# Optimization experiments

Hardware: AMD Instinct MI355X
Metric: run time of the kernel (lower is better)

Reference implementation:

```python
import jax, jax.numpy as jnp
import numpy as np

NUM_HEADS = 32
NUM_KV_HEADS = 8
HEAD_DIM = 128
HIDDEN = 4096
EPS = 1e-6
ROPE_BASE = 10000.0
NEG_INF = -1e9


def setup_inputs() -> dict:
    key = jax.random.key(0)
    ks = jax.random.split(key, 6)
    B, S = 1, 2048
    hidden_states = jax.random.normal(ks[0], (B, S, HIDDEN), dtype=jnp.float32)
    wq = jax.random.normal(ks[1], (HIDDEN, NUM_HEADS * HEAD_DIM), dtype=jnp.float32) * 0.02
    wk = jax.random.normal(ks[2], (HIDDEN, NUM_KV_HEADS * HEAD_DIM), dtype=jnp.float32) * 0.02
    wv = jax.random.normal(ks[3], (HIDDEN, NUM_KV_HEADS * HEAD_DIM), dtype=jnp.float32) * 0.02
    wo = jax.random.normal(ks[4], (NUM_HEADS * HEAD_DIM, HIDDEN), dtype=jnp.float32) * 0.02
    q_norm_w = jnp.ones((HEAD_DIM,), dtype=jnp.float32)
    k_norm_w = jnp.ones((HEAD_DIM,), dtype=jnp.float32)
    attention_mask = jnp.tril(jnp.ones((S, S), dtype=bool))[None, None]  # [1,1,S,S] causal allow-mask
    position_ids = jnp.arange(S, dtype=jnp.int64 if jax.config.jax_enable_x64 else jnp.int32)[None, :]
    return dict(hidden_states=hidden_states, wq=wq, wk=wk, wv=wv, wo=wo,
                q_norm_w=q_norm_w, k_norm_w=k_norm_w,
                attention_mask=attention_mask, position_ids=position_ids)


def _rotate_half(x):
    x1, x2 = jnp.split(x, 2, axis=-1)
    return jnp.concatenate((-x2, x1), axis=-1)


def _rms_norm(x, w):
    xf = x.astype(jnp.float32)
    var = jnp.mean(xf * xf, axis=-1, keepdims=True)
    return w * (xf * jax.lax.rsqrt(var + EPS)).astype(x.dtype)


def reference(hidden_states, wq, wk, wv, wo, q_norm_w, k_norm_w, attention_mask, position_ids):
    B, S, _ = hidden_states.shape
    dtype = hidden_states.dtype

    # projections -> [B, H, S, D]
    q = (hidden_states @ wq).reshape(B, S, NUM_HEADS, HEAD_DIM).transpose(0, 2, 1, 3)
    k = (hidden_states @ wk).reshape(B, S, NUM_KV_HEADS, HEAD_DIM).transpose(0, 2, 1, 3)
    v = (hidden_states @ wv).reshape(B, S, NUM_KV_HEADS, HEAD_DIM).transpose(0, 2, 1, 3)

    # RoPE cache (fp32), gathered by position_ids
    inv_freq = 1.0 / (ROPE_BASE ** (jnp.arange(0, HEAD_DIM, 2, dtype=jnp.float32) / HEAD_DIM))
    t = jnp.arange(S, dtype=jnp.float32)
    freqs = jnp.outer(t, inv_freq)                    # [S, D/2]
    emb = jnp.concatenate((freqs, freqs), axis=-1)    # [S, D]
    cos = jnp.cos(emb).astype(dtype)[position_ids][:, None]  # [B,1,S,D]
    sin = jnp.sin(emb).astype(dtype)[position_ids][:, None]

    q = q * cos + _rotate_half(q) * sin
    k = k * cos + _rotate_half(k) * sin

    # QK RMSNorm (after RoPE)
    q = _rms_norm(q, q_norm_w)
    k = _rms_norm(k, k_norm_w)

    # GQA repeat-kv
    n_rep = NUM_HEADS // NUM_KV_HEADS
    k = jnp.repeat(k, n_rep, axis=1)
    v = jnp.repeat(v, n_rep, axis=1)

    scores = jnp.einsum('bhqd,bhkd->bhqk', q, k) / np.sqrt(HEAD_DIM)
    scores = jnp.where(attention_mask, scores, scores + NEG_INF)
    probs = jax.nn.softmax(scores.astype(jnp.float32), axis=-1).astype(dtype)
    out = jnp.einsum('bhqk,bhkd->bhqd', probs, v)      # [B,H,S,D]
    out = out.transpose(0, 2, 1, 3).reshape(B, S, NUM_HEADS * HEAD_DIM)
    return out @ wo
```

## Files before the change

kernel.cpp:

```cpp
#include <hip/hip_runtime.h>

typedef __bf16 bf16x8 __attribute__((ext_vector_type(8)));
typedef float f32x4 __attribute__((ext_vector_type(4)));
typedef unsigned short u16x8 __attribute__((ext_vector_type(8)));
typedef unsigned short u16x4 __attribute__((ext_vector_type(4)));
typedef unsigned short u16x2 __attribute__((ext_vector_type(2)));

__device__ inline unsigned short f2bf(float f) {
    return __builtin_bit_cast(unsigned short, (__bf16)f);
}
__device__ inline float bf2f(unsigned short u) {
    return (float)__builtin_bit_cast(__bf16, u);
}

__device__ __forceinline__ float fexp2(float x) {
    float r;
    asm("v_exp_f32 %0, %1" : "=v"(r) : "v"(x));
    return r;
}

__device__ inline void storeC(float v, float* p) { *p = v; }
__device__ inline void storeC(float v, unsigned short* p) { *p = f2bf(v); }

#define MFMA16(a, b, c) __builtin_amdgcn_mfma_f32_16x16x32_bf16( \
    __builtin_bit_cast(bf16x8, a), __builtin_bit_cast(bf16x8, b), (c), 0, 0, 0)

__device__ inline void gload16(const unsigned short* g, unsigned short* l) {
    __builtin_amdgcn_global_load_lds(
        (const __attribute__((address_space(1))) unsigned int*)(g),
        (__attribute__((address_space(3))) unsigned int*)(l), 16, 0, 0);
}

__device__ __forceinline__ void bar() {
    asm volatile("" ::: "memory");
    __builtin_amdgcn_s_barrier();
    asm volatile("" ::: "memory");
}
#define WAITVM(N) asm volatile("s_waitcnt vmcnt(" #N ")" ::: "memory")

__device__ void transpose_tile128(const float* __restrict__ W,
                                  unsigned short* __restrict__ WT,
                                  int K, int N, int bx, int by,
                                  unsigned short* t_lds)
{
    constexpr int LDT = 130;
    const int kt = bx * 128, nt = by * 128;
    const int tid = threadIdx.x;
    const int c = (tid & 31) * 4;
    const int r0 = tid >> 5;
    #pragma unroll
    for (int p = 0; p < 16; ++p) {
        const int r = p * 8 + r0;
        float4 v = *(const float4*)&W[(size_t)(kt + r) * N + nt + c];
        u16x4 h;
        h[0] = f2bf(v.x); h[1] = f2bf(v.y); h[2] = f2bf(v.z); h[3] = f2bf(v.w);
        *(u16x4*)&t_lds[r * LDT + c] = h;
    }
    __syncthreads();
    const int kc = (tid >> 4) * 8;
    const int n0 = tid & 15;
    #pragma unroll
    for (int p = 0; p < 8; ++p) {
        const int n = p * 16 + n0;
        u16x8 o;
        #pragma unroll
        for (int j = 0; j < 8; ++j)
            o[j] = t_lds[(kc + j) * LDT + n];
        const int swz = (kc & 64) | ((kc & 63) ^ ((n & 7) << 3));
        *(u16x8*)&WT[(size_t)(nt + n) * K + kt + swz] = o;
    }
}

__global__ __launch_bounds__(256) void prep_all(
    const float* __restrict__ hidden, const float* __restrict__ wq,
    const float* __restrict__ wk, const float* __restrict__ wv,
    const float* __restrict__ wo, unsigned short* __restrict__ hb,
    unsigned short* __restrict__ wqt, unsigned short* __restrict__ wkt,
    unsigned short* __restrict__ wot)
{
    __shared__ __attribute__((aligned(16))) unsigned short t_lds[128 * 130];
    const int bid = blockIdx.x;
    if (bid < 4096) {
        const size_t i = ((size_t)bid * 256 + threadIdx.x) * 8;
        const size_t row7 = (i >> 12) & 7;
        float4 v0 = *(const float4*)&hidden[i];
        float4 v1 = *(const float4*)&hidden[i + 4];
        u16x8 o;
        o[0] = f2bf(v0.x); o[1] = f2bf(v0.y); o[2] = f2bf(v0.z); o[3] = f2bf(v0.w);
        o[4] = f2bf(v1.x); o[5] = f2bf(v1.y); o[6] = f2bf(v1.z); o[7] = f2bf(v1.w);
        *(u16x8*)&hb[i ^ (row7 << 3)] = o;
    } else if (bid < 5120) {
        const int tb = bid - 4096;
        transpose_tile128(wq, wqt, 4096, 4096, tb & 31, tb >> 5, t_lds);
    } else if (bid < 5376) {
        const int tb = bid - 5120;
        transpose_tile128(wk, wkt, 4096, 1024, tb & 31, tb >> 5, t_lds);
    } else if (bid < 5632) {
        const int tb = bid - 5376;
        transpose_tile128(wv, wkt + (size_t)1024 * 4096, 4096, 1024,
                          tb & 31, tb >> 5, t_lds);
    } else {
        const int tb = bid - 5632;
        transpose_tile128(wo, wot, 4096, 4096, tb & 31, tb >> 5, t_lds);
    }
}

template <typename CT, int CMODE>
__global__ __launch_bounds__(512) void gemm8(
    const unsigned short* __restrict__ A, const unsigned short* __restrict__ B,
    CT* __restrict__ C, int M, int N, int K)
{
    constexpr int ASZ = 128 * 64, BSZ = 256 * 64;
    __shared__ __attribute__((aligned(16))) unsigned short a_lds[3 * ASZ];
    __shared__ __attribute__((aligned(16))) unsigned short b_lds[3 * BSZ];

    const int bm0 = blockIdx.y * 128, bn0 = blockIdx.x * 256;
    const int tid = threadIdx.x, lane = tid & 63, wid = tid >> 6;
    const int wr = wid >> 2, wc = wid & 3;
    const int l15 = lane & 15, koff = (lane >> 4) * 8;
    const int sw = (l15 & 7) << 3;
    const int cb0 = koff ^ sw;
    const int cb1 = (32 + koff) ^ sw;

    f32x4 acc[4][4] = {};

    const size_t kbase = (CMODE == 3) ? (size_t)blockIdx.z * 2048 : 0;

    const unsigned short* ag[2];
    const unsigned short* bg[4];
    #pragma unroll
    for (int p = 0; p < 2; ++p) {
        const int row = (wid + p * 8) * 8 + (lane >> 3);
        ag[p] = A + (size_t)(bm0 + row) * K + (lane & 7) * 8 + kbase;
    }
    #pragma unroll
    for (int p = 0; p < 4; ++p) {
        const int row = (wid + p * 8) * 8 + (lane >> 3);
        bg[p] = B + (size_t)(bn0 + row) * K + (lane & 7) * 8 + kbase;
    }

    const int nt = (CMODE == 3) ? 32 : (K >> 6);

    auto stageA = [&](int s, int kt, int p) {
        gload16(ag[p] + kt, a_lds + s * ASZ + (wid + p * 8) * 512);
    };
    auto stageB = [&](int s, int kt, int p) {
        gload16(bg[p] + kt, b_lds + s * BSZ + (wid + p * 8) * 512);
    };

    #pragma unroll
    for (int p = 0; p < 2; ++p) stageA(0, 0, p);
    #pragma unroll
    for (int p = 0; p < 4; ++p) stageB(0, 0, p);
    #pragma unroll
    for (int p = 0; p < 2; ++p) stageA(1, 64, p);
    #pragma unroll
    for (int p = 0; p < 4; ++p) stageB(1, 64, p);
    WAITVM(6);
    bar();

    int sc = 0;
    for (int t = 0; t < nt; ++t) {
        const unsigned short* ab = a_lds + sc * ASZ;
        const unsigned short* bb = b_lds + sc * BSZ;
        const int ss = (sc >= 1) ? sc - 1 : 2;
        const int kt2 = (t + 2) << 6;
        const bool st = (t + 2) < nt;

        u16x8 af0, af1, af2, af3, bfr[4];

        af0 = *(const u16x8*)&ab[(wr * 64 + 0 * 16 + l15) * 64 + cb0];
        af1 = *(const u16x8*)&ab[(wr * 64 + 1 * 16 + l15) * 64 + cb0];
        af2 = *(const u16x8*)&ab[(wr * 64 + 2 * 16 + l15) * 64 + cb0];
        af3 = *(const u16x8*)&ab[(wr * 64 + 3 * 16 + l15) * 64 + cb0];
        #pragma unroll
        for (int j = 0; j < 4; ++j)
            bfr[j] = *(const u16x8*)&bb[(wc * 64 + j * 16 + l15) * 64 + cb0];
        if (st) { stageA(ss, kt2, 0); stageA(ss, kt2, 1); stageB(ss, kt2, 0); }
        bar();
        __builtin_amdgcn_s_setprio(1);
        #pragma unroll
        for (int j = 0; j < 4; ++j) {
            acc[0][j] = MFMA16(af0, bfr[j], acc[0][j]);
            acc[1][j] = MFMA16(af1, bfr[j], acc[1][j]);
            acc[2][j] = MFMA16(af2, bfr[j], acc[2][j]);
            acc[3][j] = MFMA16(af3, bfr[j], acc[3][j]);
        }
        __builtin_amdgcn_s_setprio(0);

        af0 = *(const u16x8*)&ab[(wr * 64 + 0 * 16 + l15) * 64 + cb1];
        af1 = *(const u16x8*)&ab[(wr * 64 + 1 * 16 + l15) * 64 + cb1];
        af2 = *(const u16x8*)&ab[(wr * 64 + 2 * 16 + l15) * 64 + cb1];
        af3 = *(const u16x8*)&ab[(wr * 64 + 3 * 16 + l15) * 64 + cb1];
        #pragma unroll
        for (int j = 0; j < 4; ++j)
            bfr[j] = *(const u16x8*)&bb[(wc * 64 + j * 16 + l15) * 64 + cb1];
        if (st) {
            stageB(ss, kt2, 1); stageB(ss, kt2, 2); stageB(ss, kt2, 3);
            WAITVM(6);
        } else {
            WAITVM(0);
        }
        bar();
        __builtin_amdgcn_s_setprio(1);
        #pragma unroll
        for (int j = 0; j < 4; ++j) {
            acc[0][j] = MFMA16(af0, bfr[j], acc[0][j]);
            acc[1][j] = MFMA16(af1, bfr[j], acc[1][j]);
            acc[2][j] = MFMA16(af2, bfr[j], acc[2][j]);
            acc[3][j] = MFMA16(af3, bfr[j], acc[3][j]);
        }
        __builtin_amdgcn_s_setprio(0);

        bar();
        sc = (sc == 2) ? 0 : sc + 1;
    }

    CT* Cb = C;
    if constexpr (CMODE == 3)
        Cb = C + (size_t)blockIdx.z * M * N;

    #pragma unroll
    for (int i = 0; i < 4; ++i)
        #pragma unroll
        for (int r = 0; r < 4; ++r) {
            const int row = bm0 + wr * 64 + i * 16 + (lane >> 4) * 4 + r;
            size_t base = (size_t)row * N + bn0 + wc * 64 + l15;
            #pragma unroll
            for (int j = 0; j < 4; ++j)
                storeC(acc[i][j][r], &Cb[base + j * 16]);
        }
}

__global__ __launch_bounds__(256) void combine_kv(
    const float* __restrict__ P, unsigned short* __restrict__ Kout,
    unsigned short* __restrict__ VTout)
{
    const float* P0 = P;
    const float* P1 = P + (size_t)2048 * 2048;
    const int s0 = blockIdx.y * 64, c0 = blockIdx.x * 64;
    const int tid = threadIdx.x;
    const int row = tid >> 2;
    const int cbl = (tid & 3) * 16;
    const size_t gbase = (size_t)(s0 + row) * 2048 + c0 + cbl;
    u16x8 o[2];
    #pragma unroll
    for (int j = 0; j < 2; ++j) {
        float4 a0 = *(const float4*)&P0[gbase + j * 8];
        float4 b0 = *(const float4*)&P1[gbase + j * 8];
        float4 a1 = *(const float4*)&P0[gbase + j * 8 + 4];
        float4 b1 = *(const float4*)&P1[gbase + j * 8 + 4];
        o[j][0] = f2bf(a0.x + b0.x); o[j][1] = f2bf(a0.y + b0.y);
        o[j][2] = f2bf(a0.z + b0.z); o[j][3] = f2bf(a0.w + b0.w);
        o[j][4] = f2bf(a1.x + b1.x); o[j][5] = f2bf(a1.y + b1.y);
        o[j][6] = f2bf(a1.z + b1.z); o[j][7] = f2bf(a1.w + b1.w);
    }
    if (c0 < 1024) {
        #pragma unroll
        for (int j = 0; j < 2; ++j)
            *(u16x8*)&Kout[(size_t)(s0 + row) * 1024 + c0 + cbl + j * 8] = o[j];
    } else {
        constexpr int LDT = 66;
        __shared__ unsigned short t_lds[64 * LDT];
        #pragma unroll
        for (int j = 0; j < 2; ++j)
            *(u16x8*)&t_lds[row * LDT + cbl + j * 8] = o[j];
        __syncthreads();
        const int d = row;
        #pragma unroll
        for (int j = 0; j < 2; ++j) {
            u16x8 w;
            #pragma unroll
            for (int e = 0; e < 8; ++e)
                w[e] = t_lds[(cbl + j * 8 + e) * LDT + d];
            *(u16x8*)&VTout[(size_t)(c0 - 1024 + d) * 2048 + s0 + cbl + j * 8] = w;
        }
    }
}

__device__ void rope_row(unsigned short* __restrict__ X,
                         const float* __restrict__ W,
                         float fpos, int rowstride, size_t s, int h, int t8,
                         float outscale)
{
    unsigned short* p = X + s * rowstride + h * 128 + t8 * 8;
    u16x8 lo = *(u16x8*)p;
    u16x8 hi = *(u16x8*)(p + 64);
    float na[8], nb[8];
    float ss = 0.f;
    #pragma unroll
    for (int j = 0; j < 8; ++j) {
        const int d = t8 * 8 + j;
        float inv = expf(-0.14391156831212787f * (float)d);
        float fr = fpos * inv;
        float c = cosf(fr), sn = sinf(fr);
        float a = bf2f(lo[j]), b = bf2f(hi[j]);
        na[j] = a * c - b * sn;
        nb[j] = b * c + a * sn;
        ss += na[j] * na[j] + nb[j] * nb[j];
    }
    ss += __shfl_xor(ss, 1, 8);
    ss += __shfl_xor(ss, 2, 8);
    ss += __shfl_xor(ss, 4, 8);
    const float rn = rsqrtf(ss * (1.0f / 128.0f) + 1e-6f) * outscale;
    #pragma unroll
    for (int j = 0; j < 8; ++j) {
        const int d = t8 * 8 + j;
        lo[j] = f2bf(na[j] * rn * W[d]);
        hi[j] = f2bf(nb[j] * rn * W[d + 64]);
    }
    *(u16x8*)p = lo;
    *(u16x8*)(p + 64) = hi;
}

__global__ void rope_all(unsigned short* __restrict__ Q,
                         unsigned short* __restrict__ K,
                         const int* __restrict__ pos_ids,
                         const float* __restrict__ qw,
                         const float* __restrict__ kw,
                         float qscale)
{
    const int bid = blockIdx.x;
    const int tid = threadIdx.x;
    if (bid < 2048) {
        rope_row(Q, qw, (float)pos_ids[bid], 4096, (size_t)bid,
                 tid >> 3, tid & 7, qscale);
    } else {
        const size_t s = (size_t)(bid - 2048) * 4 + (tid >> 6);
        rope_row(K, kw, (float)pos_ids[s], 1024, s,
                 (tid & 63) >> 3, tid & 7, 1.0f);
    }
}

__global__ __launch_bounds__(256, 2) void attn_kernel(
    const unsigned short* __restrict__ Q, const unsigned short* __restrict__ K,
    const unsigned short* __restrict__ VT, unsigned short* __restrict__ O)
{
    constexpr int LDK = 136, LDV = 72, LDP = 72;
    __shared__ __attribute__((aligned(16))) unsigned short k_lds[64 * LDK];
    __shared__ __attribute__((aligned(16))) unsigned short v_lds[128 * LDV];
    __shared__ __attribute__((aligned(16))) unsigned short p_lds[4 * 32 * LDP];

    const int bid = blockIdx.x;
    const int kvh = bid & 7;
    const int rest = bid >> 3;
    const int h = kvh * 4 + (rest & 3);
    const int qb = 15 - (rest >> 2);
    const int q0 = qb * 128;
    const int tid = threadIdx.x, lane = tid & 63, wid = tid >> 6;
    const int l15 = lane & 15, g4 = (lane >> 4) * 4, koff = (lane >> 4) * 8;
    const int qw = q0 + wid * 32;

    u16x8 qf[2][4];
    #pragma unroll
    for (int qt = 0; qt < 2; ++qt)
        #pragma unroll
        for (int kk = 0; kk < 4; ++kk)
            qf[qt][kk] = *(const u16x8*)&Q[(size_t)(qw + qt * 16 + l15) * 4096 +
                                           h * 128 + kk * 32 + koff];

    f32x4 o_acc[2][8] = {};
    float m_r[2] = {-1e30f, -1e30f}, l_r[2] = {0.f, 0.f};

    const int kr = tid >> 2, kd = (tid & 3) * 32;
    const int vr = tid >> 1, vc = (tid & 1) * 32;
    const unsigned short* kg = K + (size_t)kvh * 128 + kd;
    const unsigned short* vg = VT + (size_t)(kvh * 128 + vr) * 2048 + vc;

    const int nchunk = qb * 2 + 2;
    u16x8 kst[4], vst[4];
    #pragma unroll
    for (int j = 0; j < 4; ++j) {
        kst[j] = *(const u16x8*)&kg[(size_t)kr * 1024 + j * 8];
        vst[j] = *(const u16x8*)&vg[j * 8];
    }

    for (int ch = 0; ch < nchunk; ++ch) {
        const int kv0 = ch * 64;
        __syncthreads();
        #pragma unroll
        for (int j = 0; j < 4; ++j) {
            *(u16x8*)&k_lds[kr * LDK + kd + j * 8] = kst[j];
            *(u16x8*)&v_lds[vr * LDV + vc + j * 8] = vst[j];
        }
        __syncthreads();
        if (ch + 1 < nchunk) {
            const int kv1 = kv0 + 64;
            #pragma unroll
            for (int j = 0; j < 4; ++j) {
                kst[j] = *(const u16x8*)&kg[(size_t)(kv1 + kr) * 1024 + j * 8];
                vst[j] = *(const u16x8*)&vg[kv1 + j * 8];
            }
        }

        if (kv0 <= qw + 31) {
            f32x4 sacc[2][4] = {};
            #pragma unroll
            for (int kk = 0; kk < 4; ++kk)
                #pragma unroll
                for (int jt = 0; jt < 4; ++jt) {
                    u16x8 kf = *(u16x8*)&k_lds[(jt * 16 + l15) * LDK + kk * 32 + koff];
                    #pragma unroll
                    for (int qt = 0; qt < 2; ++qt)
                        sacc[qt][jt] = MFMA16(kf, qf[qt][kk], sacc[qt][jt]);
                }

            const bool needmask = (kv0 + 63 > qw);
            #pragma unroll
            for (int qt = 0; qt < 2; ++qt) {
                const int q = qw + qt * 16 + l15;
                if (needmask) {
                    #pragma unroll
                    for (int jt = 0; jt < 4; ++jt)
                        #pragma unroll
                        for (int r = 0; r < 4; ++r)
                            if (kv0 + jt * 16 + g4 + r > q) sacc[qt][jt][r] = -1e9f;
                }
                float pmax = sacc[qt][0][0];
                #pragma unroll
                for (int jt = 0; jt < 4; ++jt)
                    #pragma unroll
                    for (int r = 0; r < 4; ++r)
                        pmax = fmaxf(pmax, sacc[qt][jt][r]);
                pmax = fmaxf(pmax, __shfl_xor(pmax, 16));
                pmax = fmaxf(pmax, __shfl_xor(pmax, 32));
                if (__any(pmax > m_r[qt] + 11.5415603f)) {
                    float mnew = fmaxf(m_r[qt], pmax);
                    float alpha = fexp2(m_r[qt] - mnew);
                    m_r[qt] = mnew;
                    l_r[qt] *= alpha;
                    float arow[4];
                    #pragma unroll
                    for (int r = 0; r < 4; ++r)
                        arow[r] = __shfl(alpha, g4 + r, 16);
                    #pragma unroll
                    for (int nt = 0; nt < 8; ++nt)
                        #pragma unroll
                        for (int r = 0; r < 4; ++r)
                            o_acc[qt][nt][r] *= arow[r];
                }
                float ps = 0.f;
                #pragma unroll
                for (int jt = 0; jt < 4; ++jt)
                    #pragma unroll
                    for (int r = 0; r < 4; ++r) {
                        float e = fexp2(sacc[qt][jt][r] - m_r[qt]);
                        sacc[qt][jt][r] = e;
                        ps += e;
                    }
                ps += __shfl_xor(ps, 16);
                ps += __shfl_xor(ps, 32);
                l_r[qt] += ps;
                const int prow = (wid * 32 + qt * 16 + l15) * LDP;
                #pragma unroll
                for (int jt = 0; jt < 4; ++jt) {
                    u16x4 w;
                    #pragma unroll
                    for (int r = 0; r < 4; ++r) w[r] = f2bf(sacc[qt][jt][r]);
                    *(u16x4*)&p_lds[prow + jt * 16 + g4] = w;
                }
            }

            u16x8 pf[2][2];
            #pragma unroll
            for (int qt = 0; qt < 2; ++qt)
                #pragma unroll
                for (int ks = 0; ks < 2; ++ks)
                    pf[qt][ks] = *(u16x8*)&p_lds[(wid * 32 + qt * 16 + l15) * LDP +
                                                 ks * 32 + koff];
            #pragma unroll
            for (int nt = 0; nt < 8; ++nt)
                #pragma unroll
                for (int ks = 0; ks < 2; ++ks) {
                    u16x8 vf = *(u16x8*)&v_lds[(nt * 16 + l15) * LDV + ks * 32 + koff];
                    #pragma unroll
                    for (int qt = 0; qt < 2; ++qt)
                        o_acc[qt][nt] = MFMA16(pf[qt][ks], vf, o_acc[qt][nt]);
                }
        }
    }

    #pragma unroll
    for (int qt = 0; qt < 2; ++qt) {
        float lrow[4];
        #pragma unroll
        for (int r = 0; r < 4; ++r)
            lrow[r] = __shfl(l_r[qt], g4 + r, 16);
        #pragma unroll
        for (int r = 0; r < 4; ++r) {
            float inv_l = 1.0f / lrow[r];
            int row = qw + qt * 16 + g4 + r;
            const int r7s = (row & 7) << 3;
            #pragma unroll
            for (int nt = 0; nt < 8; ++nt) {
                int col = h * 128 + nt * 16 + l15;
                O[(size_t)row * 4096 + (col ^ r7s)] =
                    f2bf(o_acc[qt][nt][r] * inv_l);
            }
        }
    }
}

extern "C" void kernel_launch(void* const* d_in, const int* in_sizes, int n_in,
                              void* d_out, int out_size, void* d_ws, size_t ws_size,
                              hipStream_t stream)
{
    (void)in_sizes; (void)n_in; (void)out_size; (void)ws_size;
    const float* hidden = (const float*)d_in[0];
    const float* wq     = (const float*)d_in[1];
    const float* wk     = (const float*)d_in[2];
    const float* wv     = (const float*)d_in[3];
    const float* wo     = (const float*)d_in[4];
    const float* qnw    = (const float*)d_in[5];
    const float* knw    = (const float*)d_in[6];
    const int*   pos    = (const int*)d_in[8];
    float* out = (float*)d_out;

    const size_t MB = 1024 * 1024;
    char* ws = (char*)d_ws;
    unsigned short* q_ws  = (unsigned short*)(ws);
    unsigned short* k_ws  = (unsigned short*)(ws + 16 * MB);
    unsigned short* vt_ws = (unsigned short*)(ws + 20 * MB);
    unsigned short* hb    = (unsigned short*)(ws + 24 * MB);
    unsigned short* a_ws  = hb;
    unsigned short* wqt   = (unsigned short*)(ws + 40 * MB);
    float*          kvP   = (float*)(ws + 40 * MB);
    unsigned short* wkt   = (unsigned short*)(ws + 72 * MB);
    unsigned short* wot   = (unsigned short*)(ws + 88 * MB);

    prep_all<<<6656, 256, 0, stream>>>(hidden, wq, wk, wv, wo,
                                       hb, wqt, wkt, wot);

    gemm8<unsigned short, 0><<<dim3(16, 16), 512, 0, stream>>>(
        hb, wqt, q_ws, 2048, 4096, 4096);
    gemm8<float, 3><<<dim3(8, 16, 2), 512, 0, stream>>>(
        hb, wkt, kvP, 2048, 2048, 4096);
    combine_kv<<<dim3(32, 32), 256, 0, stream>>>(kvP, k_ws, vt_ws);

    rope_all<<<2560, 256, 0, stream>>>(q_ws, k_ws, pos, qnw, knw,
                                       0.12751743341633942f);

    attn_kernel<<<512, 256, 0, stream>>>(q_ws, k_ws, vt_ws, a_ws);

    gemm8<float, 0><<<dim3(16, 16), 512, 0, stream>>>(
        a_ws, wot, out, 2048, 4096, 4096);
}
```

Measured before the change: 327.1 us.

## Use 256x256 split-K GEMM with partial-sum combine kernels for projections

Adds a new GEMM kernel with 256x256 output tiles, double-buffered LDS and two blocks per CU. It splits K across blockIdx.z and writes fp32 partial sums, which separate combine kernels reduce into bf16 Q, K/V^T, or the fp32 output. The larger tiles raise arithmetic intensity, and split-K supplies enough blocks to fill the CUs. The cost is extra fp32 partial-sum traffic, additional launches, and a dependence on workspace size, with a fallback to the old path when the workspace is too small.

```diff
diff --git a/kernel.cpp b/kernel.cpp
--- a/kernel.cpp
+++ b/kernel.cpp
@@ -102,6 +102,172 @@
     } else {
         const int tb = bid - 5632;
         transpose_tile128(wo, wot, 4096, 4096, tb & 31, tb >> 5, t_lds);
+    }
+}
+
+__global__ __launch_bounds__(512, 2) void gemm256(
+    const unsigned short* __restrict__ A, const unsigned short* __restrict__ B,
+    float* __restrict__ P, int M, int N, int K)
+{
+    constexpr int TSZ = 256 * 64;
+    __shared__ __attribute__((aligned(16))) unsigned short a_lds[2 * TSZ];
+    __shared__ __attribute__((aligned(16))) unsigned short b_lds[2 * TSZ];
+
+    const int bm0 = blockIdx.y * 256, bn0 = blockIdx.x * 256;
+    const int tid = threadIdx.x, lane = tid & 63, wid = tid >> 6;
+    const int wr = wid >> 2, wc = wid & 3;
+    const int l15 = lane & 15, koff = (lane >> 4) * 8;
+    const int sw = (l15 & 7) << 3;
+    const int cb0 = koff ^ sw, cb1 = (32 + koff) ^ sw;
+
+    f32x4 acc[8][4] = {};
+
+    const size_t kbase = (size_t)blockIdx.z * K;
+    const int r8 = tid >> 3, c8 = (tid & 7) * 8;
+    const unsigned short* ag = A + (size_t)(bm0 + r8) * 4096 + c8 + kbase;
+    const unsigned short* bg = B + (size_t)(bn0 + r8) * 4096 + c8 + kbase;
+
+    auto stage = [&](int bf, int kt) {
+        unsigned short* ab = a_lds + bf * TSZ;
+        unsigned short* bb = b_lds + bf * TSZ;
+        #pragma unroll
+        for (int p = 0; p < 4; ++p)
+            gload16(ag + (size_t)(p * 64) * 4096 + kt, ab + p * 4096 + wid * 512);
+        #pragma unroll
+        for (int p = 0; p < 4; ++p)
+            gload16(bg + (size_t)(p * 64) * 4096 + kt, bb + p * 4096 + wid * 512);
+    };
+
+    const int nt = K >> 6;
+    stage(0, 0);
+    WAITVM(0);
+    bar();
+
+    for (int t = 0; t < nt; ++t) {
+        const int buf = t & 1;
+        const unsigned short* ab = a_lds + buf * TSZ;
+        const unsigned short* bb = b_lds + buf * TSZ;
+        u16x8 af[8], bf4[4];
+
+        #pragma unroll
+        for (int i = 0; i < 8; ++i)
+            af[i] = *(const u16x8*)&ab[(wr * 128 + i * 16 + l15) * 64 + cb0];
+        #pragma unroll
+        for (int j = 0; j < 4; ++j)
+            bf4[j] = *(const u16x8*)&bb[(wc * 64 + j * 16 + l15) * 64 + cb0];
+        if (t + 1 < nt) stage(buf ^ 1, (t + 1) << 6);
+        bar();
+        __builtin_amdgcn_s_setprio(1);
+        #pragma unroll
+        for (int i = 0; i < 8; ++i)
+            #pragma unroll
+            for (int j = 0; j < 4; ++j)
+                acc[i][j] = MFMA16(af[i], bf4[j], acc[i][j]);
+        __builtin_amdgcn_s_setprio(0);
+
+        #pragma unroll
+        for (int i = 0; i < 8; ++i)
+            af[i] = *(const u16x8*)&ab[(wr * 128 + i * 16 + l15) * 64 + cb1];
+        #pragma unroll
+        for (int j = 0; j < 4; ++j)
+            bf4[j] = *(const u16x8*)&bb[(wc * 64 + j * 16 + l15) * 64 + cb1];
+        WAITVM(0);
+        bar();
+        __builtin_amdgcn_s_setprio(1);
+        #pragma unroll
+        for (int i = 0; i < 8; ++i)
+            #pragma unroll
+            for (int j = 0; j < 4; ++j)
+                acc[i][j] = MFMA16(af[i], bf4[j], acc[i][j]);
+        __builtin_amdgcn_s_setprio(0);
+
+        bar();
+    }
+
+    float* Pz = P + (size_t)blockIdx.z * M * N;
+    #pragma unroll
+    for (int i = 0; i < 8; ++i)
+        #pragma unroll
+        for (int r = 0; r < 4; ++r) {
+            const int row = bm0 + wr * 128 + i * 16 + (lane >> 4) * 4 + r;
+            size_t base = (size_t)row * N + bn0 + wc * 64 + l15;
+            #pragma unroll
+            for (int j = 0; j < 4; ++j)
+                Pz[base + j * 16] = acc[i][j][r];
+        }
+}
+
+__global__ __launch_bounds__(256) void combine2_bf16(
+    const float* __restrict__ P, unsigned short* __restrict__ Y, size_t n)
+{
+    const size_t i = ((size_t)blockIdx.x * 256 + threadIdx.x) * 8;
+    const float* P1 = P + n;
+    u16x8 o;
+    #pragma unroll
+    for (int j = 0; j < 8; j += 4) {
+        float4 a = *(const float4*)&P[i + j];
+        float4 b = *(const float4*)&P1[i + j];
+        o[j + 0] = f2bf(a.x + b.x); o[j + 1] = f2bf(a.y + b.y);
+        o[j + 2] = f2bf(a.z + b.z); o[j + 3] = f2bf(a.w + b.w);
+    }
+    *(u16x8*)&Y[i] = o;
+}
+
+__global__ __launch_bounds__(256) void combine2_f32(
+    const float* __restrict__ P, float* __restrict__ Y, size_t n)
+{
+    const size_t i = ((size_t)blockIdx.x * 256 + threadIdx.x) * 4;
+    float4 a = *(const float4*)&P[i];
+    float4 b = *(const float4*)&P[i + n];
+    float4 o;
+    o.x = a.x + b.x; o.y = a.y + b.y; o.z = a.z + b.z; o.w = a.w + b.w;
+    *(float4*)&Y[i] = o;
+}
+
+__global__ __launch_bounds__(256) void combine_kv4(
+    const float* __restrict__ P, unsigned short* __restrict__ Kout,
+    unsigned short* __restrict__ VTout)
+{
+    const int s0 = blockIdx.y * 64, c0 = blockIdx.x * 64;
+    const int tid = threadIdx.x;
+    const int row = tid >> 2;
+    const int cbl = (tid & 3) * 16;
+    const size_t gbase = (size_t)(s0 + row) * 2048 + c0 + cbl;
+    const size_t zs = (size_t)2048 * 2048;
+    u16x8 o[2];
+    #pragma unroll
+    for (int j = 0; j < 2; ++j) {
+        float s[8] = {};
+        #pragma unroll
+        for (int z = 0; z < 4; ++z) {
+            float4 a = *(const float4*)&P[z * zs + gbase + j * 8];
+            float4 b = *(const float4*)&P[z * zs + gbase + j * 8 + 4];
+            s[0] += a.x; s[1] += a.y; s[2] += a.z; s[3] += a.w;
+            s[4] += b.x; s[5] += b.y; s[6] += b.z; s[7] += b.w;
+        }
+        #pragma unroll
+        for (int e = 0; e < 8; ++e) o[j][e] = f2bf(s[e]);
+    }
+    if (c0 < 1024) {
+        #pragma unroll
+        for (int j = 0; j < 2; ++j)
+            *(u16x8*)&Kout[(size_t)(s0 + row) * 1024 + c0 + cbl + j * 8] = o[j];
+    } else {
+        constexpr int LDT = 66;
+        __shared__ unsigned short t_lds[64 * LDT];
+        #pragma unroll
+        for (int j = 0; j < 2; ++j)
+            *(u16x8*)&t_lds[row * LDT + cbl + j * 8] = o[j];
+        __syncthreads();
+        const int d = row;
+        #pragma unroll
+        for (int j = 0; j < 2; ++j) {
+            u16x8 w;
+            #pragma unroll
+            for (int e = 0; e < 8; ++e)
+                w[e] = t_lds[(cbl + j * 8 + e) * LDT + d];
+            *(u16x8*)&VTout[(size_t)(c0 - 1024 + d) * 2048 + s0 + cbl + j * 8] = w;
+        }
     }
 }
 
@@ -505,7 +671,7 @@
                               void* d_out, int out_size, void* d_ws, size_t ws_size,
                               hipStream_t stream)
 {
-    (void)in_sizes; (void)n_in; (void)out_size; (void)ws_size;
+    (void)in_sizes; (void)n_in; (void)out_size;
     const float* hidden = (const float*)d_in[0];
     const float* wq     = (const float*)d_in[1];
     const float* wk     = (const float*)d_in[2];
@@ -527,21 +693,40 @@
     float*          kvP   = (float*)(ws + 40 * MB);
     unsigned short* wkt   = (unsigned short*)(ws + 72 * MB);
     unsigned short* wot   = (unsigned short*)(ws + 88 * MB);
+    float*          Ppart = (float*)(ws + 120 * MB);
 
     prep_all<<<6656, 256, 0, stream>>>(hidden, wq, wk, wv, wo,
                                        hb, wqt, wkt, wot);
 
-    gemm8<unsigned short, 0><<<dim3(16, 16), 512, 0, stream>>>(
-        hb, wqt, q_ws, 2048, 4096, 4096);
-    gemm8<float, 3><<<dim3(8, 16, 2), 512, 0, stream>>>(
-        hb, wkt, kvP, 2048, 2048, 4096);
-    combine_kv<<<dim3(32, 32), 256, 0, stream>>>(kvP, k_ws, vt_ws);
-
-    rope_all<<<2560, 256, 0, stream>>>(q_ws, k_ws, pos, qnw, knw,
-                                       0.12751743341633942f);
-
-    attn_kernel<<<512, 256, 0, stream>>>(q_ws, k_ws, vt_ws, a_ws);
-
-    gemm8<float, 0><<<dim3(16, 16), 512, 0, stream>>>(
-        a_ws, wot, out, 2048, 4096, 4096);
-}
+    if (ws_size >= (size_t)184 * MB) {
+        gemm256<<<dim3(16, 8, 2), 512, 0, stream>>>(
+            hb, wqt, Ppart, 2048, 4096, 2048);
+        combine2_bf16<<<4096, 256, 0, stream>>>(
+            Ppart, q_ws, (size_t)2048 * 4096);
+        gemm256<<<dim3(8, 8, 4), 512, 0, stream>>>(
+            hb, wkt, Ppart, 2048, 2048, 1024);
+        combine_kv4<<<dim3(32, 32), 256, 0, stream>>>(Ppart, k_ws, vt_ws);
+
+        rope_all<<<2560, 256, 0, stream>>>(q_ws, k_ws, pos, qnw, knw,
+                                           0.12751743341633942f);
+        attn_kernel<<<512, 256, 0, stream>>>(q_ws, k_ws, vt_ws, a_ws);
+
+        gemm256<<<dim3(16, 8, 2), 512, 0, stream>>>(
+            a_ws, wot, Ppart, 2048, 4096, 2048);
+        combine2_f32<<<8192, 256, 0, stream>>>(
+            Ppart, out, (size_t)2048 * 4096);
+    } else {
+        gemm8<unsigned short, 0><<<dim3(16, 16), 512, 0, stream>>>(
+            hb, wqt, q_ws, 2048, 4096, 4096);
+        gemm8<float, 3><<<dim3(8, 16, 2), 512, 0, stream>>>(
+            hb, wkt, kvP, 2048, 2048, 4096);
+        combine_kv<<<dim3(32, 32), 256, 0, stream>>>(kvP, k_ws, vt_ws);
+
+        rope_all<<<2560, 256, 0, stream>>>(q_ws, k_ws, pos, qnw, knw,
+                                           0.12751743341633942f);
+        attn_kernel<<<512, 256, 0, stream>>>(q_ws, k_ws, vt_ws, a_ws);
+
+        gemm8<float, 0><<<dim3(16, 16), 512, 0, stream>>>(
+            a_ws, wot, out, 2048, 4096, 4096);
+    }
+}
```

Measured after the change: 370.7 us. 13.3% more time.
